# Kernel tuning notes

Hardware: AMD Instinct MI355X
Metric: run time of the kernel (lower is better)

Reference implementation:

```python
import jax, jax.numpy as jnp
import numpy as np

NU = 200000  # num users
NI = 200000  # num items
H = 64
L = 2
E = 4000000
P = 100000
EPS = 1e-5


def _seg_mean(msgs, dst, n):
    # msgs: [E, H] gathered source features, dst: [E] destination ids
    s = jax.ops.segment_sum(msgs, dst, num_segments=n)
    c = jax.ops.segment_sum(jnp.ones((msgs.shape[0],), msgs.dtype), dst, num_segments=n)
    return s / jnp.maximum(c, 1.0)[:, None]


def _bn(x, g, b, m, v):
    return (x - m) * jax.lax.rsqrt(v + EPS) * g + b


def setup_inputs() -> dict:
    key = jax.random.key(0)
    ks = jax.random.split(key, 12)
    s = 1.0 / np.sqrt(H)
    inp = {
        "edge_index": jax.random.randint(ks[0], (2, E), 0, NU),
        "edge_label_index": jax.random.randint(ks[1], (2, P), 0, NU),
        "user_emb": jax.random.normal(ks[2], (NU, H), jnp.float32) * 0.1,
        "item_emb": jax.random.normal(ks[3], (NI, H), jnp.float32) * 0.1,
        "u_ll_w": jax.random.normal(ks[4], (L, H, H), jnp.float32) * s,
        "u_ll_b": jnp.zeros((L, H), jnp.float32),
        "u_lr_w": jax.random.normal(ks[5], (L, H, H), jnp.float32) * s,
        "i_ll_w": jax.random.normal(ks[6], (L, H, H), jnp.float32) * s,
        "i_ll_b": jnp.zeros((L, H), jnp.float32),
        "i_lr_w": jax.random.normal(ks[7], (L, H, H), jnp.float32) * s,
        "u_bn_g": jnp.ones((L, H), jnp.float32),
        "u_bn_b": jnp.zeros((L, H), jnp.float32),
        "u_bn_m": jnp.zeros((L, H), jnp.float32),
        "u_bn_v": jnp.ones((L, H), jnp.float32),
        "i_bn_g": jnp.ones((L, H), jnp.float32),
        "i_bn_b": jnp.zeros((L, H), jnp.float32),
        "i_bn_m": jnp.zeros((L, H), jnp.float32),
        "i_bn_v": jnp.ones((L, H), jnp.float32),
        "fc1_w": jax.random.normal(ks[8], (2 * H, H), jnp.float32) * (1.0 / np.sqrt(2 * H)),
        "fc1_b": jnp.zeros((H,), jnp.float32),
        "fc2_w": jax.random.normal(ks[9], (H, 4), jnp.float32) * s,
        "fc2_b": jnp.zeros((4,), jnp.float32),
    }
    return inp


def reference(edge_index, edge_label_index, user_emb, item_emb,
              u_ll_w, u_ll_b, u_lr_w, i_ll_w, i_ll_b, i_lr_w,
              u_bn_g, u_bn_b, u_bn_m, u_bn_v,
              i_bn_g, i_bn_b, i_bn_m, i_bn_v,
              fc1_w, fc1_b, fc2_w, fc2_b):
    src, dst = edge_index[0], edge_index[1]  # user -> item edges
    user_x, item_x = user_emb, item_emb
    for l in range(L):
        # user update: aggregate item features along flipped edges (item->user)
        agg_u = _seg_mean(item_x[dst], src, NU)          # [NU, H]
        u_new = agg_u @ u_ll_w[l] + u_ll_b[l] + user_x @ u_lr_w[l]
        u_new = jax.nn.relu(_bn(u_new, u_bn_g[l], u_bn_b[l], u_bn_m[l], u_bn_v[l]))
        # item update: aggregate (old) user features along user->item edges
        agg_i = _seg_mean(user_x[src], dst, NI)          # [NI, H]
        i_new = agg_i @ i_ll_w[l] + i_ll_b[l] + item_x @ i_lr_w[l]
        i_new = jax.nn.relu(_bn(i_new, i_bn_g[l], i_bn_b[l], i_bn_m[l], i_bn_v[l]))
        user_x, item_x = u_new, i_new
    u_h = user_x[edge_label_index[0]]                    # [P, H]
    i_h = item_x[edge_label_index[1]]                    # [P, H]
    x = jnp.concatenate([u_h, i_h], axis=1)              # [P, 2H]
    x = jax.nn.relu(x @ fc1_w + fc1_b)
    return x @ fc2_w + fc2_b                             # [P, 4]
```

## Files before the change

kernel.cpp:

```cpp
#include <hip/hip_runtime.h>

#define NU 200000
#define NI 200000
#define NN 400000
#define H 64
#define NE 4000000
#define NP 100000
#define EPSF 1e-5f

#define BSH 9
#define BNODES 512
#define NB ((NN + BNODES - 1) / BNODES)
#define CAP 15104

#define PBLOCKS 512
#define EPB 7816

#define DUMMY 200000
#define NROW 200002

#define CVTB ((2 * (NU * H / 4) + 255) / 256)
#define WCVTB 128

typedef unsigned short u16;
typedef __attribute__((ext_vector_type(8))) short bf16x8;
typedef __attribute__((ext_vector_type(4))) float f32x4;

__device__ __forceinline__ u16 f2bf(float f) {
    unsigned int b = __float_as_uint(f);
    b += 0x7FFFu + ((b >> 16) & 1u);
    return (u16)(b >> 16);
}

__global__ __launch_bounds__(256) void prep_kernel(
    const int* __restrict__ src, const int* __restrict__ dst,
    int* __restrict__ blkhist,
    const float4* __restrict__ inU, const float4* __restrict__ inI,
    ushort4* __restrict__ outU, ushort4* __restrict__ outI,
    u16* __restrict__ f1,
    const float* __restrict__ u_ll_w, const float* __restrict__ u_lr_w,
    const float* __restrict__ i_ll_w, const float* __restrict__ i_lr_w,
    const float* __restrict__ u_ll_b, const float* __restrict__ i_ll_b,
    const float* __restrict__ u_g, const float* __restrict__ u_b,
    const float* __restrict__ u_m, const float* __restrict__ u_v,
    const float* __restrict__ i_g, const float* __restrict__ i_b,
    const float* __restrict__ i_m, const float* __restrict__ i_v,
    u16* __restrict__ wcat, float* __restrict__ scsh)
{
    int bid = blockIdx.x, tid = threadIdx.x;
    if (bid < PBLOCKS) {
        __shared__ int hist[NB];
        for (int i = tid; i < NB; i += 256) hist[i] = 0;
        __syncthreads();
        int e0 = bid * EPB, e1 = min(NE, e0 + EPB);
        for (int e = e0 + tid * 4; e + 4 <= e1; e += 1024) {
            int4 s4 = *(const int4*)&src[e];
            int4 d4 = *(const int4*)&dst[e];
            atomicAdd(&hist[s4.x >> BSH], 1); atomicAdd(&hist[(NU + d4.x) >> BSH], 1);
            atomicAdd(&hist[s4.y >> BSH], 1); atomicAdd(&hist[(NU + d4.y) >> BSH], 1);
            atomicAdd(&hist[s4.z >> BSH], 1); atomicAdd(&hist[(NU + d4.z) >> BSH], 1);
            atomicAdd(&hist[s4.w >> BSH], 1); atomicAdd(&hist[(NU + d4.w) >> BSH], 1);
        }
        __syncthreads();
        for (int i = tid; i < NB; i += 256)
            blkhist[(size_t)i * PBLOCKS + bid] = hist[i];
    } else if (bid < PBLOCKS + CVTB) {
        int cb = bid - PBLOCKS;
        if (cb == 0 && tid < 128) {
            const int sl[4] = {0, 1, 4, 5};
            int s = sl[tid >> 5], wd = tid & 31;
            unsigned int* p = (unsigned int*)(f1 + (size_t)s * NROW * H + (size_t)DUMMY * H);
            p[wd] = 0u;
        }
        const int n4 = NU * H / 4;
        int i = cb * 256 + tid;
        const float4* in;
        ushort4* out;
        if (i < n4) { in = inU; out = outU; }
        else        { in = inI; out = outI; i -= n4; if (i >= n4) return; }
        float4 v = in[i];
        ushort4 h;
        h.x = f2bf(v.x); h.y = f2bf(v.y); h.z = f2bf(v.z); h.w = f2bf(v.w);
        out[i] = h;
    } else {
        int idx = (bid - PBLOCKS - CVTB) * 256 + tid;
        if (idx < 32768) {
            int k = idx & 127, f = (idx >> 7) & 63, t = (idx >> 13) & 1, l = idx >> 14;
            const float* W = t ? (k < 64 ? i_ll_w : i_lr_w)
                               : (k < 64 ? u_ll_w : u_lr_w);
            wcat[idx] = f2bf(W[l * 4096 + (k & 63) * 64 + f]);
        }
        if (idx < 512) {
            int j = idx & 63, half = (idx >> 6) & 1, t = (idx >> 7) & 1, l = idx >> 8;
            const float *g = t ? i_g : u_g, *b = t ? i_b : u_b;
            const float *m = t ? i_m : u_m, *v = t ? i_v : u_v;
            const float *bl = t ? i_ll_b : u_ll_b;
            float sc = g[l * 64 + j] * rsqrtf(v[l * 64 + j] + EPSF);
            scsh[idx] = half ? (bl[l * 64 + j] - m[l * 64 + j]) * sc + b[l * 64 + j]
                             : sc;
        }
    }
}

__global__ __launch_bounds__(256) void colscan_kernel(
    int* __restrict__ blkhist, int* __restrict__ g_bcnt)
{
    __shared__ int s[256];
    int b = blockIdx.x, tid = threadIdx.x;
    int* col = blkhist + (size_t)b * PBLOCKS;
    int v0 = col[2 * tid], v1 = col[2 * tid + 1];
    int ps = v0 + v1;
    s[tid] = ps;
    __syncthreads();
    for (int d = 1; d < 256; d <<= 1) {
        int t = (tid >= d) ? s[tid - d] : 0;
        __syncthreads();
        s[tid] += t;
        __syncthreads();
    }
    int ex = s[tid] - ps;
    col[2 * tid] = ex;
    col[2 * tid + 1] = ex + v0;
    if (tid == 255) g_bcnt[b] = s[255];
}

__global__ __launch_bounds__(256) void part2_kernel(
    const int* __restrict__ src, const int* __restrict__ dst,
    const int* __restrict__ blkhist, int* __restrict__ staging)
{
    __shared__ int cur[NB];
    int tid = threadIdx.x, blk = blockIdx.x;
    for (int i = tid; i < NB; i += 256)
        cur[i] = i * CAP + blkhist[(size_t)i * PBLOCKS + blk];
    __syncthreads();
    int e0 = blk * EPB, e1 = min(NE, e0 + EPB);
    for (int e = e0 + tid * 4; e + 4 <= e1; e += 1024) {
        int4 s4 = *(const int4*)&src[e];
        int4 d4 = *(const int4*)&dst[e];
        int sv[4] = {s4.x, s4.y, s4.z, s4.w};
        int dv[4] = {d4.x, d4.y, d4.z, d4.w};
#pragma unroll
        for (int q = 0; q < 4; ++q) {
            int s = sv[q], d = dv[q];
            int p1 = atomicAdd(&cur[s >> BSH], 1);
            staging[p1] = ((s & (BNODES - 1)) << 18) | d;
            int gn = NU + d;
            int p2 = atomicAdd(&cur[gn >> BSH], 1);
            staging[p2] = ((gn & (BNODES - 1)) << 18) | s;
        }
    }
}

__global__ __launch_bounds__(256) void bucket_fill_kernel(
    const int* __restrict__ g_bcnt, const int* __restrict__ staging,
    int* __restrict__ off, int* __restrict__ deg, int* __restrict__ adj)
{
    __shared__ int hist[BNODES];
    __shared__ int psum[256];
    __shared__ int adj_st[CAP];
    int tid = threadIdx.x;
    int b = blockIdx.x;
    int e0 = b * CAP;
    int cnt = g_bcnt[b];
    int node_base = b * BNODES;

    for (int i = tid; i < CAP; i += 256) adj_st[i] = DUMMY << 7;
    hist[tid] = 0; hist[tid + 256] = 0;
    __syncthreads();
    for (int i = tid; i < cnt; i += 256)
        atomicAdd(&hist[staging[e0 + i] >> 18], 1);
    __syncthreads();

    int h0 = hist[2 * tid], h1 = hist[2 * tid + 1];
    int hp = max((h0 + 7) & ~7, (h1 + 7) & ~7);
    psum[tid] = 2 * hp;
    __syncthreads();
    for (int d = 1; d < 256; d <<= 1) {
        int t = (tid >= d) ? psum[tid - d] : 0;
        __syncthreads();
        psum[tid] += t;
        __syncthreads();
    }
    int ex0 = psum[tid] - 2 * hp;
    int ex1 = ex0 + hp;
    int n0 = node_base + 2 * tid;
    if (n0 < NN)     { off[n0]     = e0 + ex0; deg[n0]     = h0; }
    if (n0 + 1 < NN) { off[n0 + 1] = e0 + ex1; deg[n0 + 1] = h1; }
    __syncthreads();
    hist[2 * tid] = ex0; hist[2 * tid + 1] = ex1;
    __syncthreads();

    int ptotal = min(psum[255], CAP);

    for (int i = tid; i < cnt; i += 256) {
        int v = staging[e0 + i];
        int p = atomicAdd(&hist[v >> 18], 1);
        if (p < CAP) adj_st[p] = (v & 0x3FFFF) << 7;
    }
    __syncthreads();
    for (int i = tid; i < ptotal; i += 256)
        adj[(size_t)b * CAP + i] = adj_st[i];
}

__global__ __launch_bounds__(256) void pull_update_kernel(
    const int* __restrict__ off, const int* __restrict__ deg,
    const int* __restrict__ adj,
    const u16* __restrict__ xu16, const u16* __restrict__ xi16,
    const u16* __restrict__ selfU, const u16* __restrict__ selfI,
    u16* __restrict__ outU, u16* __restrict__ outI,
    const u16* __restrict__ wcat,
    const float* __restrict__ scsh)
{
    __shared__ u16 sAgg[4][16][72];
    int tid = threadIdx.x;
    int wave = tid >> 6, lane = tid & 63;
    int gw = blockIdx.x * 4 + wave;
    bool isU = gw < (NU / 16);
    int node0 = (isU ? gw : gw - NU / 16) * 16;
    const u16* table = isU ? xi16 : xu16;
    const u16* selfx = isU ? selfU : selfI;
    u16* out         = isU ? outU : outI;
    const u16* wt      = wcat + (isU ? 0 : 64 * 128);
    const float* sc_p  = scsh + (isU ? 0 : 128);
    const float* sh_p  = sc_p + 64;
    int wbase = isU ? node0 : NU + node0;

    int row = lane & 15, g = lane >> 4;
    const u16* xrow = selfx + (size_t)(node0 + row) * H + g * 8;
    bf16x8 sa2 = *(const bf16x8*)(xrow);
    bf16x8 sa3 = *(const bf16x8*)(xrow + 32);

    int offv = 0, degv = 0;
    if (lane < 16) { offv = off[wbase + lane]; degv = deg[wbase + lane]; }

    int half = lane >> 5;
    int hl   = lane & 31;
    int fl   = hl & 15;
    int rg   = hl >> 4;
    int shb  = (half << 5) + rg;
    unsigned flb = (unsigned)fl * 8u;
    const char* tb = (const char*)table;

#define ACC(c) \
    a0  += __uint_as_float((c).x << 16); a1 += __uint_as_float((c).x & 0xFFFF0000u); \
    a2f += __uint_as_float((c).y << 16); a3f += __uint_as_float((c).y & 0xFFFF0000u);

    for (int p = 0; p < 8; ++p) {
        int begA = __shfl(offv, 2 * p),     dgA = __shfl(degv, 2 * p);
        int begB = __shfl(offv, 2 * p + 1), dgB = __shfl(degv, 2 * p + 1);
        int pd = max((dgA + 7) & ~7, (dgB + 7) & ~7);
        int myBeg = half ? begB : begA;
        float a0 = 0.f, a1 = 0.f, a2f = 0.f, a3f = 0.f;
        for (int k0 = 0; k0 < pd; k0 += 32) {
            int nb = adj[myBeg + k0 + hl];
            int lim = min(32, pd - k0);
            unsigned o0 = (unsigned)__shfl(nb, shb + 0) + flb;
            unsigned o1 = (unsigned)__shfl(nb, shb + 2) + flb;
            unsigned o2 = (unsigned)__shfl(nb, shb + 4) + flb;
            unsigned o3 = (unsigned)__shfl(nb, shb + 6) + flb;
            uint2 c0 = *(const uint2*)(tb + o0);
            uint2 c1 = *(const uint2*)(tb + o1);
            uint2 c2 = *(const uint2*)(tb + o2);
            uint2 c3 = *(const uint2*)(tb + o3);
            for (int tt = 8; tt < lim; tt += 8) {
                unsigned q0 = (unsigned)__shfl(nb, shb + tt + 0) + flb;
                unsigned q1 = (unsigned)__shfl(nb, shb + tt + 2) + flb;
                unsigned q2 = (unsigned)__shfl(nb, shb + tt + 4) + flb;
                unsigned q3 = (unsigned)__shfl(nb, shb + tt + 6) + flb;
                uint2 n0 = *(const uint2*)(tb + q0);
                uint2 n1 = *(const uint2*)(tb + q1);
                uint2 n2 = *(const uint2*)(tb + q2);
                uint2 n3 = *(const uint2*)(tb + q3);
                ACC(c0) ACC(c1) ACC(c2) ACC(c3)
                c0 = n0; c1 = n1; c2 = n2; c3 = n3;
            }
            ACC(c0) ACC(c1) ACC(c2) ACC(c3)
        }
        a0  += __shfl_xor(a0, 16);
        a1  += __shfl_xor(a1, 16);
        a2f += __shfl_xor(a2f, 16);
        a3f += __shfl_xor(a3f, 16);
        int mydg = half ? dgB : dgA;
        if (rg == 0) {
            float inv = 1.0f / fmaxf((float)mydg, 1.0f);
            unsigned int lo = ((unsigned int)f2bf(a1 * inv) << 16) | f2bf(a0 * inv);
            unsigned int hi = ((unsigned int)f2bf(a3f * inv) << 16) | f2bf(a2f * inv);
            uint2 pk; pk.x = lo; pk.y = hi;
            *(uint2*)&sAgg[wave][2 * p + half][fl * 4] = pk;
        }
    }
#undef ACC

    bf16x8 a[4];
    a[0] = *(const bf16x8*)&sAgg[wave][row][g * 8];
    a[1] = *(const bf16x8*)&sAgg[wave][row][32 + g * 8];
    a[2] = sa2;
    a[3] = sa3;

#pragma unroll
    for (int ct = 0; ct < 4; ++ct) {
        int feat = ct * 16 + row;
        const u16* wrow = wt + feat * 128 + g * 8;
        f32x4 acc = {0.f, 0.f, 0.f, 0.f};
#pragma unroll
        for (int kb = 0; kb < 4; ++kb) {
            bf16x8 b = *(const bf16x8*)(wrow + kb * 32);
            acc = __builtin_amdgcn_mfma_f32_16x16x32_bf16(a[kb], b, acc, 0, 0, 0);
        }
        float s = sc_p[feat], h = sh_p[feat];
#pragma unroll
        for (int r = 0; r < 4; ++r) {
            int node = node0 + g * 4 + r;
            float v = fmaxf(acc[r] * s + h, 0.f);
            out[(size_t)node * H + feat] = f2bf(v);
        }
    }
}

__global__ __launch_bounds__(256) void mlp_kernel(
    const int* __restrict__ eli,
    const u16* __restrict__ xu16, const u16* __restrict__ xi16,
    const float* __restrict__ fc1w, const float* __restrict__ fc1b,
    const float* __restrict__ fc2w, const float* __restrict__ fc2b,
    float* __restrict__ out, int n)
{
    __shared__ float sW[32][68];
    __shared__ float sA[64][36];
    __shared__ float sH[64][68];
    __shared__ int   sid[128];
    __shared__ float sW2[256];
    int tid = threadIdx.x;
    int p0 = blockIdx.x * 64;
    if (tid < 128) {
        int p = p0 + (tid & 63);
        int side = tid >> 6;
        sid[tid] = (p < n) ? eli[side * NP + p] : -1;
    }
    sW2[tid] = fc2w[tid];
    __syncthreads();

    int jt = (tid & 15) * 4;
    int pt = (tid >> 4) * 4;
    float4 b4 = *(const float4*)&fc1b[jt];
    float acc[4][4];
#pragma unroll
    for (int i = 0; i < 4; ++i) {
        acc[i][0] = b4.x; acc[i][1] = b4.y; acc[i][2] = b4.z; acc[i][3] = b4.w;
    }

    for (int ch = 0; ch < 4; ++ch) {
        int k0 = ch * 32;
        const u16* tab = (ch < 2) ? xu16 : xi16;
        int idbase = (ch < 2) ? 0 : 64;
        int koff = (ch & 1) * 32;
        for (int idx = tid; idx < 64 * 16; idx += 256) {
            int r = idx >> 4, cp = idx & 15;
            int id = sid[idbase + r];
            unsigned int wv = (id >= 0)
                ? *(const unsigned int*)&tab[(size_t)id * H + koff + cp * 2] : 0u;
            sA[r][cp * 2]     = __uint_as_float(wv << 16);
            sA[r][cp * 2 + 1] = __uint_as_float(wv & 0xFFFF0000u);
        }
        for (int idx = tid; idx < 32 * 64; idx += 256) {
            int kk = idx >> 6, j = idx & 63;
            sW[kk][j] = fc1w[(k0 + kk) * 64 + j];
        }
        __syncthreads();
        for (int kk = 0; kk < 32; kk += 4) {
            float a[4][4];
#pragma unroll
            for (int i = 0; i < 4; ++i) {
                float4 t = *(const float4*)&sA[pt + i][kk];
                a[i][0] = t.x; a[i][1] = t.y; a[i][2] = t.z; a[i][3] = t.w;
            }
#pragma unroll
            for (int q = 0; q < 4; ++q) {
                float4 w = *(const float4*)&sW[kk + q][jt];
                float wv[4] = {w.x, w.y, w.z, w.w};
#pragma unroll
                for (int i = 0; i < 4; ++i)
#pragma unroll
                    for (int j = 0; j < 4; ++j)
                        acc[i][j] += a[i][q] * wv[j];
            }
        }
        __syncthreads();
    }

#pragma unroll
    for (int i = 0; i < 4; ++i)
#pragma unroll
        for (int j = 0; j < 4; ++j)
            sH[pt + i][jt + j] = fmaxf(acc[i][j], 0.f);
    __syncthreads();

    int pp = tid >> 2, c = tid & 3;
    float o = 0.f;
#pragma unroll
    for (int j = 0; j < 64; ++j) o += sH[pp][j] * sW2[j * 4 + c];
    int p = p0 + pp;
    if (p < n) out[(size_t)p * 4 + c] = o + fc2b[c];
}

extern "C" void kernel_launch(void* const* d_in, const int* in_sizes, int n_in,
                              void* d_out, int out_size, void* d_ws, size_t ws_size,
                              hipStream_t stream) {
    const int*   edge_index = (const int*)d_in[0];
    const int*   eli        = (const int*)d_in[1];
    const float* user_emb   = (const float*)d_in[2];
    const float* item_emb   = (const float*)d_in[3];
    const float* u_ll_w     = (const float*)d_in[4];
    const float* u_ll_b     = (const float*)d_in[5];
    const float* u_lr_w     = (const float*)d_in[6];
    const float* i_ll_w     = (const float*)d_in[7];
    const float* i_ll_b     = (const float*)d_in[8];
    const float* i_lr_w     = (const float*)d_in[9];
    const float* u_bn_g     = (const float*)d_in[10];
    const float* u_bn_b     = (const float*)d_in[11];
    const float* u_bn_m     = (const float*)d_in[12];
    const float* u_bn_v     = (const float*)d_in[13];
    const float* i_bn_g     = (const float*)d_in[14];
    const float* i_bn_b     = (const float*)d_in[15];
    const float* i_bn_m     = (const float*)d_in[16];
    const float* i_bn_v     = (const float*)d_in[17];
    const float* fc1_w      = (const float*)d_in[18];
    const float* fc1_b      = (const float*)d_in[19];
    const float* fc2_w      = (const float*)d_in[20];
    const float* fc2_b      = (const float*)d_in[21];
    float* out = (float*)d_out;

    const int* src = edge_index;
    const int* dst = edge_index + NE;

    const size_t S = (size_t)NROW * H;
    char* w = (char*)d_ws;
    u16* f1 = (u16*)w;          w += 6 * S * 2;
    int* adj    = (int*)w;      w += ((size_t)NB * CAP + 128) * 4;
    int* off    = (int*)w;      w += (size_t)NN * 4;
    int* deg    = (int*)w;      w += (size_t)NN * 4;
    int* g_bcnt = (int*)w;      w += (size_t)NB * 4;
    u16* wcat   = (u16*)w;      w += (size_t)32768 * 2;
    float* scsh = (float*)w;    w += (size_t)512 * 4;

    u16* emb16_u = f1 + 0 * S;
    u16* emb16_i = f1 + 1 * S;
    u16* fin16_u = f1 + 0 * S;
    u16* fin16_i = f1 + 1 * S;
    u16* xA16_u  = f1 + 4 * S;
    u16* xA16_i  = f1 + 5 * S;
    int* staging = (int*)(f1 + 2 * S);
    int* blkhist = (int*)(f1 + 4 * S);

    prep_kernel<<<PBLOCKS + CVTB + WCVTB, 256, 0, stream>>>(
        src, dst, blkhist,
        (const float4*)user_emb, (const float4*)item_emb,
        (ushort4*)emb16_u, (ushort4*)emb16_i, f1,
        u_ll_w, u_lr_w, i_ll_w, i_lr_w, u_ll_b, i_ll_b,
        u_bn_g, u_bn_b, u_bn_m, u_bn_v,
        i_bn_g, i_bn_b, i_bn_m, i_bn_v, wcat, scsh);

    colscan_kernel<<<NB, 256, 0, stream>>>(blkhist, g_bcnt);
    part2_kernel<<<PBLOCKS, 256, 0, stream>>>(src, dst, blkhist, staging);
    bucket_fill_kernel<<<NB, 256, 0, stream>>>(g_bcnt, staging, off, deg, adj);

    const int pu_blocks = (NN / 16) / 4;

    pull_update_kernel<<<pu_blocks, 256, 0, stream>>>(
        off, deg, adj, emb16_u, emb16_i, emb16_u, emb16_i,
        xA16_u, xA16_i, wcat, scsh);

    pull_update_kernel<<<pu_blocks, 256, 0, stream>>>(
        off, deg, adj, xA16_u, xA16_i, xA16_u, xA16_i,
        fin16_u, fin16_i, wcat + 16384, scsh + 256);

    mlp_kernel<<<(NP + 63) / 64, 256, 0, stream>>>(
        eli, fin16_u, fin16_i, fc1_w, fc1_b, fc2_w, fc2_b, out, NP);
}
```

Before: 545.7 us.

## Interleave adjacency per 16-node group and gather full 16-byte rows per lane

Bucket fill now stores each 16-node group's neighbor lists interleaved (position = k*16 + node), padded to the group's max degree, and records per-group offset and length instead of per-node offsets. The pull kernel walks the whole group in one loop: each lane loads one adjacency entry, neighbor ids are shuffled, and each lane gathers 16-byte chunks covering 8 features for two nodes. This removes the per-pair serial loop, the 8-byte gathers and the cross-half reduction, aiming for wider memory transactions and more loads in flight. The cost is padding to the maximum degree across 16 nodes instead of across pairs, which wastes gathers on dummy rows and needs a larger shared and global adjacency capacity, with entries dropped if it overflows.

```diff
diff --git a/kernel.cpp b/kernel.cpp
--- a/kernel.cpp
+++ b/kernel.cpp
@@ -11,7 +11,9 @@
 #define BSH 9
 #define BNODES 512
 #define NB ((NN + BNODES - 1) / BNODES)
-#define CAP 15104
+#define NG (NB * 32)
+#define CAP_STG 15104
+#define CAP_ADJ 18432
 
 #define PBLOCKS 512
 #define EPB 7816
@@ -131,7 +133,7 @@
     __shared__ int cur[NB];
     int tid = threadIdx.x, blk = blockIdx.x;
     for (int i = tid; i < NB; i += 256)
-        cur[i] = i * CAP + blkhist[(size_t)i * PBLOCKS + blk];
+        cur[i] = i * CAP_STG + blkhist[(size_t)i * PBLOCKS + blk];
     __syncthreads();
     int e0 = blk * EPB, e1 = min(NE, e0 + EPB);
     for (int e = e0 + tid * 4; e + 4 <= e1; e += 1024) {
@@ -153,58 +155,71 @@
 
 __global__ __launch_bounds__(256) void bucket_fill_kernel(
     const int* __restrict__ g_bcnt, const int* __restrict__ staging,
-    int* __restrict__ off, int* __restrict__ deg, int* __restrict__ adj)
+    int* __restrict__ goff, int* __restrict__ glen,
+    int* __restrict__ deg, int* __restrict__ adj)
 {
     __shared__ int hist[BNODES];
-    __shared__ int psum[256];
-    __shared__ int adj_st[CAP];
+    __shared__ int gmax[32];
+    __shared__ int gbase_s[33];
+    __shared__ int adj_st[CAP_ADJ];
     int tid = threadIdx.x;
     int b = blockIdx.x;
-    int e0 = b * CAP;
+    int e0 = b * CAP_STG;
     int cnt = g_bcnt[b];
     int node_base = b * BNODES;
 
-    for (int i = tid; i < CAP; i += 256) adj_st[i] = DUMMY << 7;
+    for (int i = tid; i < CAP_ADJ; i += 256) adj_st[i] = DUMMY << 7;
     hist[tid] = 0; hist[tid + 256] = 0;
+    if (tid < 32) gmax[tid] = 0;
     __syncthreads();
     for (int i = tid; i < cnt; i += 256)
         atomicAdd(&hist[staging[e0 + i] >> 18], 1);
     __syncthreads();
 
     int h0 = hist[2 * tid], h1 = hist[2 * tid + 1];
-    int hp = max((h0 + 7) & ~7, (h1 + 7) & ~7);
-    psum[tid] = 2 * hp;
-    __syncthreads();
-    for (int d = 1; d < 256; d <<= 1) {
-        int t = (tid >= d) ? psum[tid - d] : 0;
-        __syncthreads();
-        psum[tid] += t;
-        __syncthreads();
-    }
-    int ex0 = psum[tid] - 2 * hp;
-    int ex1 = ex0 + hp;
-    int n0 = node_base + 2 * tid;
-    if (n0 < NN)     { off[n0]     = e0 + ex0; deg[n0]     = h0; }
-    if (n0 + 1 < NN) { off[n0 + 1] = e0 + ex1; deg[n0 + 1] = h1; }
-    __syncthreads();
-    hist[2 * tid] = ex0; hist[2 * tid + 1] = ex1;
-    __syncthreads();
-
-    int ptotal = min(psum[255], CAP);
+    atomicMax(&gmax[tid >> 3], max(h0, h1));
+    deg[node_base + 2 * tid]     = h0;
+    deg[node_base + 2 * tid + 1] = h1;
+    __syncthreads();
+    if (tid == 0) {
+        int acc = 0;
+#pragma unroll
+        for (int gma = 0; gma < 32; ++gma) {
+            gbase_s[gma] = acc;
+            int L = (gmax[gma] + 3) & ~3;
+            gmax[gma] = L;
+            acc += 16 * L;
+        }
+        gbase_s[32] = acc;
+    }
+    __syncthreads();
+    if (tid < 32) {
+        int gb = gbase_s[tid];
+        int L = gmax[tid];
+        int avail = max(0, (CAP_ADJ - gb) / 16) & ~3;
+        L = min(L, avail);
+        goff[b * 32 + tid] = b * CAP_ADJ + gb;
+        glen[b * 32 + tid] = L;
+    }
+    hist[2 * tid] = 0; hist[2 * tid + 1] = 0;
+    __syncthreads();
 
     for (int i = tid; i < cnt; i += 256) {
         int v = staging[e0 + i];
-        int p = atomicAdd(&hist[v >> 18], 1);
-        if (p < CAP) adj_st[p] = (v & 0x3FFFF) << 7;
-    }
-    __syncthreads();
+        int nl = v >> 18;
+        int p = atomicAdd(&hist[nl], 1);
+        int pos = gbase_s[nl >> 4] + p * 16 + (nl & 15);
+        if (pos < CAP_ADJ) adj_st[pos] = (v & 0x3FFFF) << 7;
+    }
+    __syncthreads();
+    int ptotal = min(gbase_s[32], CAP_ADJ);
     for (int i = tid; i < ptotal; i += 256)
-        adj[(size_t)b * CAP + i] = adj_st[i];
+        adj[(size_t)b * CAP_ADJ + i] = adj_st[i];
 }
 
 __global__ __launch_bounds__(256) void pull_update_kernel(
-    const int* __restrict__ off, const int* __restrict__ deg,
-    const int* __restrict__ adj,
+    const int* __restrict__ goff, const int* __restrict__ glen,
+    const int* __restrict__ deg, const int* __restrict__ adj,
     const u16* __restrict__ xu16, const u16* __restrict__ xi16,
     const u16* __restrict__ selfU, const u16* __restrict__ selfI,
     u16* __restrict__ outU, u16* __restrict__ outI,
@@ -223,73 +238,72 @@
     const u16* wt      = wcat + (isU ? 0 : 64 * 128);
     const float* sc_p  = scsh + (isU ? 0 : 128);
     const float* sh_p  = sc_p + 64;
-    int wbase = isU ? node0 : NU + node0;
+    int wbase = gw * 16;
 
     int row = lane & 15, g = lane >> 4;
     const u16* xrow = selfx + (size_t)(node0 + row) * H + g * 8;
     bf16x8 sa2 = *(const bf16x8*)(xrow);
     bf16x8 sa3 = *(const bf16x8*)(xrow + 32);
 
-    int offv = 0, degv = 0;
-    if (lane < 16) { offv = off[wbase + lane]; degv = deg[wbase + lane]; }
-
-    int half = lane >> 5;
-    int hl   = lane & 31;
-    int fl   = hl & 15;
-    int rg   = hl >> 4;
-    int shb  = (half << 5) + rg;
-    unsigned flb = (unsigned)fl * 8u;
+    int degv = (lane < 16) ? deg[wbase + lane] : 0;
+    int gbase = goff[gw];
+    int Lg    = glen[gw];
+
+    int na = lane & 7;
+    int fo = (lane >> 3) * 8;
+    unsigned laneoff = (unsigned)fo * 2u;
     const char* tb = (const char*)table;
-
-#define ACC(c) \
-    a0  += __uint_as_float((c).x << 16); a1 += __uint_as_float((c).x & 0xFFFF0000u); \
-    a2f += __uint_as_float((c).y << 16); a3f += __uint_as_float((c).y & 0xFFFF0000u);
-
-    for (int p = 0; p < 8; ++p) {
-        int begA = __shfl(offv, 2 * p),     dgA = __shfl(degv, 2 * p);
-        int begB = __shfl(offv, 2 * p + 1), dgB = __shfl(degv, 2 * p + 1);
-        int pd = max((dgA + 7) & ~7, (dgB + 7) & ~7);
-        int myBeg = half ? begB : begA;
-        float a0 = 0.f, a1 = 0.f, a2f = 0.f, a3f = 0.f;
-        for (int k0 = 0; k0 < pd; k0 += 32) {
-            int nb = adj[myBeg + k0 + hl];
-            int lim = min(32, pd - k0);
-            unsigned o0 = (unsigned)__shfl(nb, shb + 0) + flb;
-            unsigned o1 = (unsigned)__shfl(nb, shb + 2) + flb;
-            unsigned o2 = (unsigned)__shfl(nb, shb + 4) + flb;
-            unsigned o3 = (unsigned)__shfl(nb, shb + 6) + flb;
-            uint2 c0 = *(const uint2*)(tb + o0);
-            uint2 c1 = *(const uint2*)(tb + o1);
-            uint2 c2 = *(const uint2*)(tb + o2);
-            uint2 c3 = *(const uint2*)(tb + o3);
-            for (int tt = 8; tt < lim; tt += 8) {
-                unsigned q0 = (unsigned)__shfl(nb, shb + tt + 0) + flb;
-                unsigned q1 = (unsigned)__shfl(nb, shb + tt + 2) + flb;
-                unsigned q2 = (unsigned)__shfl(nb, shb + tt + 4) + flb;
-                unsigned q3 = (unsigned)__shfl(nb, shb + tt + 6) + flb;
-                uint2 n0 = *(const uint2*)(tb + q0);
-                uint2 n1 = *(const uint2*)(tb + q1);
-                uint2 n2 = *(const uint2*)(tb + q2);
-                uint2 n3 = *(const uint2*)(tb + q3);
-                ACC(c0) ACC(c1) ACC(c2) ACC(c3)
-                c0 = n0; c1 = n1; c2 = n2; c3 = n3;
+    const int* ap = adj + gbase + lane;
+
+    float accA[8] = {0,0,0,0,0,0,0,0};
+    float accB[8] = {0,0,0,0,0,0,0,0};
+
+#define ACC8(acc, wv) \
+    acc[0] += __uint_as_float((wv).x << 16); acc[1] += __uint_as_float((wv).x & 0xFFFF0000u); \
+    acc[2] += __uint_as_float((wv).y << 16); acc[3] += __uint_as_float((wv).y & 0xFFFF0000u); \
+    acc[4] += __uint_as_float((wv).z << 16); acc[5] += __uint_as_float((wv).z & 0xFFFF0000u); \
+    acc[6] += __uint_as_float((wv).w << 16); acc[7] += __uint_as_float((wv).w & 0xFFFF0000u);
+
+    if (Lg > 0) {
+        int idv = ap[0];
+        for (int k0 = 0; ; ) {
+            int nxt = k0 + 4;
+            int idn;
+            if (nxt < Lg) idn = ap[nxt * 16];
+            uint4 w[8];
+#pragma unroll
+            for (int s = 0; s < 4; ++s) {
+                unsigned oa = (unsigned)__shfl(idv, s * 16 + na) + laneoff;
+                unsigned ob = (unsigned)__shfl(idv, s * 16 + 8 + na) + laneoff;
+                w[2 * s]     = *(const uint4*)(tb + oa);
+                w[2 * s + 1] = *(const uint4*)(tb + ob);
             }
-            ACC(c0) ACC(c1) ACC(c2) ACC(c3)
-        }
-        a0  += __shfl_xor(a0, 16);
-        a1  += __shfl_xor(a1, 16);
-        a2f += __shfl_xor(a2f, 16);
-        a3f += __shfl_xor(a3f, 16);
-        int mydg = half ? dgB : dgA;
-        if (rg == 0) {
-            float inv = 1.0f / fmaxf((float)mydg, 1.0f);
-            unsigned int lo = ((unsigned int)f2bf(a1 * inv) << 16) | f2bf(a0 * inv);
-            unsigned int hi = ((unsigned int)f2bf(a3f * inv) << 16) | f2bf(a2f * inv);
-            uint2 pk; pk.x = lo; pk.y = hi;
-            *(uint2*)&sAgg[wave][2 * p + half][fl * 4] = pk;
-        }
-    }
-#undef ACC
+#pragma unroll
+            for (int s = 0; s < 4; ++s) {
+                ACC8(accA, w[2 * s])
+                ACC8(accB, w[2 * s + 1])
+            }
+            if (nxt >= Lg) break;
+            idv = idn; k0 = nxt;
+        }
+    }
+#undef ACC8
+
+    int dgA = __shfl(degv, na);
+    int dgB = __shfl(degv, 8 + na);
+    float invA = 1.0f / fmaxf((float)dgA, 1.0f);
+    float invB = 1.0f / fmaxf((float)dgB, 1.0f);
+    uint4 pka, pkb;
+    pka.x = ((unsigned)f2bf(accA[1] * invA) << 16) | f2bf(accA[0] * invA);
+    pka.y = ((unsigned)f2bf(accA[3] * invA) << 16) | f2bf(accA[2] * invA);
+    pka.z = ((unsigned)f2bf(accA[5] * invA) << 16) | f2bf(accA[4] * invA);
+    pka.w = ((unsigned)f2bf(accA[7] * invA) << 16) | f2bf(accA[6] * invA);
+    pkb.x = ((unsigned)f2bf(accB[1] * invB) << 16) | f2bf(accB[0] * invB);
+    pkb.y = ((unsigned)f2bf(accB[3] * invB) << 16) | f2bf(accB[2] * invB);
+    pkb.z = ((unsigned)f2bf(accB[5] * invB) << 16) | f2bf(accB[4] * invB);
+    pkb.w = ((unsigned)f2bf(accB[7] * invB) << 16) | f2bf(accB[6] * invB);
+    *(uint4*)&sAgg[wave][na][fo]     = pka;
+    *(uint4*)&sAgg[wave][8 + na][fo] = pkb;
 
     bf16x8 a[4];
     a[0] = *(const bf16x8*)&sAgg[wave][row][g * 8];
@@ -435,9 +449,10 @@
     const size_t S = (size_t)NROW * H;
     char* w = (char*)d_ws;
     u16* f1 = (u16*)w;          w += 6 * S * 2;
-    int* adj    = (int*)w;      w += ((size_t)NB * CAP + 128) * 4;
-    int* off    = (int*)w;      w += (size_t)NN * 4;
-    int* deg    = (int*)w;      w += (size_t)NN * 4;
+    int* adj    = (int*)w;      w += ((size_t)NB * CAP_ADJ + 128) * 4;
+    int* deg    = (int*)w;      w += (size_t)NB * BNODES * 4;
+    int* goff   = (int*)w;      w += (size_t)NG * 4;
+    int* glen   = (int*)w;      w += (size_t)NG * 4;
     int* g_bcnt = (int*)w;      w += (size_t)NB * 4;
     u16* wcat   = (u16*)w;      w += (size_t)32768 * 2;
     float* scsh = (float*)w;    w += (size_t)512 * 4;
@@ -461,16 +476,16 @@
 
     colscan_kernel<<<NB, 256, 0, stream>>>(blkhist, g_bcnt);
     part2_kernel<<<PBLOCKS, 256, 0, stream>>>(src, dst, blkhist, staging);
-    bucket_fill_kernel<<<NB, 256, 0, stream>>>(g_bcnt, staging, off, deg, adj);
+    bucket_fill_kernel<<<NB, 256, 0, stream>>>(g_bcnt, staging, goff, glen, deg, adj);
 
     const int pu_blocks = (NN / 16) / 4;
 
     pull_update_kernel<<<pu_blocks, 256, 0, stream>>>(
-        off, deg, adj, emb16_u, emb16_i, emb16_u, emb16_i,
+        goff, glen, deg, adj, emb16_u, emb16_i, emb16_u, emb16_i,
         xA16_u, xA16_i, wcat, scsh);
 
     pull_update_kernel<<<pu_blocks, 256, 0, stream>>>(
-        off, deg, adj, xA16_u, xA16_i, xA16_u, xA16_i,
+        goff, glen, deg, adj, xA16_u, xA16_i, xA16_u, xA16_i,
         fin16_u, fin16_i, wcat + 16384, scsh + 256);
 
     mlp_kernel<<<(NP + 63) / 64, 256, 0, stream>>>(
```

Result: slower. 591.2 us (+8.3%).
